# Performance work log

Hardware: AMD Instinct MI355X
Metric: run time of the kernel (lower is better)

## Reference

```python
import jax, jax.numpy as jnp
import numpy as np

MIN_NORM = 1e-15
PROJ_EPS = 4e-3  # fp32 eps used by hgcn PoincareBall


def _artanh(x):
    x = jnp.clip(x, -1.0 + 1e-7, 1.0 - 1e-7)
    return 0.5 * jnp.log((1.0 + x) / (1.0 - x))


def _norm(x):
    return jnp.maximum(jnp.linalg.norm(x, axis=-1, keepdims=True), MIN_NORM)


def proj(x, c):
    norm = _norm(x)
    maxnorm = (1.0 - PROJ_EPS) / jnp.sqrt(c)
    return jnp.where(norm > maxnorm, x / norm * maxnorm, x)


def expmap0(u, c):
    sqrt_c = jnp.sqrt(c)
    u_norm = _norm(u)
    return jnp.tanh(sqrt_c * u_norm) * u / (sqrt_c * u_norm)


def logmap0(p, c):
    sqrt_c = jnp.sqrt(c)
    p_norm = _norm(p)
    return _artanh(sqrt_c * p_norm) * p / (sqrt_c * p_norm)


def mobius_add(x, y, c):
    x2 = jnp.sum(x * x, axis=-1, keepdims=True)
    y2 = jnp.sum(y * y, axis=-1, keepdims=True)
    xy = jnp.sum(x * y, axis=-1, keepdims=True)
    num = (1.0 + 2.0 * c * xy + c * y2) * x + (1.0 - c * x2) * y
    denom = 1.0 + 2.0 * c * xy + c * c * x2 * y2
    return num / jnp.maximum(denom, MIN_NORM)


def mobius_matvec(m, x, c):
    sqrt_c = jnp.sqrt(c)
    x_norm = _norm(x)
    mx = x @ m.T  # [N, out]
    mx_norm = _norm(mx)
    res_c = jnp.tanh(mx_norm / x_norm * _artanh(sqrt_c * x_norm)) * mx / (mx_norm * sqrt_c)
    cond = jnp.all(mx == 0.0, axis=-1, keepdims=True)
    return jnp.where(cond, jnp.zeros_like(res_c), res_c)


def setup_inputs() -> dict:
    key = jax.random.key(0)
    k1, k2, k3 = jax.random.split(key, 3)
    N, D = 8192, 256
    c = 1.0
    x = 0.05 * jax.random.normal(k1, (N, D), dtype=jnp.float32)
    x = proj(x, c)  # valid points on the Poincare ball
    # sparse-ish row-normalized adjacency, materialized densely
    a = (jax.random.uniform(k2, (N, N)) < 0.004).astype(jnp.float32)
    a = a + jnp.eye(N, dtype=jnp.float32)
    adj = a / jnp.sum(a, axis=-1, keepdims=True)
    gain = np.sqrt(2.0)
    bound = gain * np.sqrt(6.0 / (D + D))  # xavier_uniform with gain sqrt(2)
    weight = jax.random.uniform(k3, (D, D), minval=-bound, maxval=bound, dtype=jnp.float32)
    bias = jnp.zeros((D,), dtype=jnp.float32)
    return {"x": x, "adj": adj, "weight": weight, "bias": bias}


def reference(x, adj, weight, bias):
    c_in = jnp.float32(1.0)
    c_out = jnp.float32(1.0)
    # HypLinear (dropout=0, eval mode)
    mv = mobius_matvec(weight, x, c_in)
    res = proj(mv, c_in)
    hyp_bias = proj(expmap0(bias[None, :], c_in), c_in)  # proj_tan0 is identity
    h = proj(mobius_add(res, hyp_bias, c_in), c_in)
    # HypAgg (use_att=False): tangent-space neighborhood aggregation
    x_tangent = logmap0(h, c_in)
    support_t = adj @ x_tangent
    h = proj(expmap0(support_t, c_in), c_in)
    # HypAct
    xt = jax.nn.relu(logmap0(h, c_in))
    h = proj(expmap0(xt, c_out), c_out)
    return (h, adj)
```

## Files before the change

### kernel.cpp

```cpp
#include <hip/hip_runtime.h>
#include <hip/hip_bf16.h>

#define N_NODES 8192
#define D_DIM   256

typedef __attribute__((ext_vector_type(8))) short short8v;
typedef __attribute__((ext_vector_type(4))) float f32x4;

__device__ __forceinline__ float artanh_clip(float x) {
    x = fminf(x, 1.0f - 1e-7f);
    return 0.5f * logf((1.0f + x) / (1.0f - x));
}

__device__ __forceinline__ ushort4 cvt4_bf16(float4 v) {
    ushort4 b;
    b.x = __bfloat16_as_ushort(__float2bfloat16(v.x));
    b.y = __bfloat16_as_ushort(__float2bfloat16(v.y));
    b.z = __bfloat16_as_ushort(__float2bfloat16(v.z));
    b.w = __bfloat16_as_ushort(__float2bfloat16(v.w));
    return b;
}

__global__ void k0_bias(const float* __restrict__ bias, float* __restrict__ hbg) {
    __shared__ float sp[4];
    __shared__ float s_g;
    int t = threadIdx.x;
    float u = bias[t];
    float v = u * u;
    #pragma unroll
    for (int o = 1; o < 64; o <<= 1) v += __shfl_xor(v, o);
    if ((t & 63) == 0) sp[t >> 6] = v;
    __syncthreads();
    if (t == 0) {
        float s  = sp[0] + sp[1] + sp[2] + sp[3];
        float un = fmaxf(sqrtf(s), 1e-15f);
        float t1 = tanhf(un);
        s_g = (t1 > 0.996f) ? (0.996f / un) : (t1 / un);
    }
    __syncthreads();
    float hb = s_g * u;
    hbg[t] = hb;
    float v2 = hb * hb;
    #pragma unroll
    for (int o = 1; o < 64; o <<= 1) v2 += __shfl_xor(v2, o);
    if ((t & 63) == 0) sp[t >> 6] = v2;
    __syncthreads();
    if (t == 0) hbg[256] = sp[0] + sp[1] + sp[2] + sp[3];
}

__global__ __launch_bounds__(256) void k1_hyplinear(
    const float* __restrict__ x, const float* __restrict__ W,
    const float* __restrict__ hbg, __hip_bfloat16* __restrict__ xtT)
{
    __shared__ __align__(16) float sx[32][260];
    __shared__ __align__(16) float sw[256][68];
    __shared__ float s_xn[32], s_P[32], s_Q[32];
    __shared__ float s_hb[256];
    __shared__ float s_b2;

    const int t  = threadIdx.x;
    const int r0 = blockIdx.x * 32;

    {
        int row = t >> 3, c0 = (t & 7) * 32;
        const float4* src = (const float4*)(x + (r0 + row) * 256 + c0);
        float4* dst = (float4*)(&sx[row][c0]);
        #pragma unroll
        for (int i = 0; i < 8; i++) dst[i] = src[i];
    }
    s_hb[t] = hbg[t];
    if (t == 0) s_b2 = hbg[256];
    __syncthreads();

    {
        int r = t >> 3, j = t & 7;
        float s2 = 0.f;
        #pragma unroll
        for (int i = 0; i < 32; i++) { float v = sx[r][j * 32 + i]; s2 += v * v; }
        s2 += __shfl_xor(s2, 1); s2 += __shfl_xor(s2, 2); s2 += __shfl_xor(s2, 4);
        if (j == 0) s_xn[r] = s2;
    }

    float acc[32];
    #pragma unroll
    for (int r = 0; r < 32; r++) acc[r] = 0.f;

    for (int kc = 0; kc < 4; kc++) {
        __syncthreads();
        int d0 = t >> 4, j4 = (t & 15) * 4;
        #pragma unroll
        for (int i = 0; i < 16; i++) {
            int d = d0 + i * 16;
            float4 w4 = *(const float4*)(W + d * 256 + kc * 64 + j4);
            *(float4*)(&sw[d][j4]) = w4;
        }
        __syncthreads();
        #pragma unroll
        for (int kk = 0; kk < 16; kk++) {
            float4 w4 = *(const float4*)(&sw[t][kk * 4]);
            #pragma unroll
            for (int r = 0; r < 32; r++) {
                float4 x4 = *(const float4*)(&sx[r][kc * 64 + kk * 4]);
                acc[r] += w4.x * x4.x + w4.y * x4.y + w4.z * x4.z + w4.w * x4.w;
            }
        }
    }
    __syncthreads();
    #pragma unroll
    for (int r = 0; r < 32; r++) sx[r][t] = acc[r];
    __syncthreads();

    {
        int r = t >> 3, j = t & 7;
        float s2 = 0.f, dt = 0.f;
        #pragma unroll
        for (int i = 0; i < 32; i++) {
            float v = sx[r][j * 32 + i];
            s2 += v * v;
            dt += v * s_hb[j * 32 + i];
        }
        s2 += __shfl_xor(s2, 1); s2 += __shfl_xor(s2, 2); s2 += __shfl_xor(s2, 4);
        dt += __shfl_xor(dt, 1); dt += __shfl_xor(dt, 2); dt += __shfl_xor(dt, 4);
        if (j == 0) {
            float b2  = s_b2;
            float xn  = fmaxf(sqrtf(s_xn[r]), 1e-15f);
            float mx2 = s2;
            float mxn = fmaxf(sqrtf(mx2), 1e-15f);
            float at = artanh_clip(xn);
            float tt = tanhf(mxn / xn * at);
            float fr = tt / mxn;
            if (tt > 0.996f) fr = 0.996f / mxn;
            float mvn = fminf(tt, 0.996f);
            float x2  = mvn * mvn;
            float xy  = fr * dt;
            float cA  = 1.0f + 2.0f * xy + b2;
            float cB  = 1.0f - x2;
            float den = fmaxf(1.0f + 2.0f * xy + x2 * b2, 1e-15f);
            float P0 = cA * fr / den;
            float Q0 = cB / den;
            float hn = sqrtf(fmaxf(P0 * P0 * mx2 + 2.0f * P0 * Q0 * dt + Q0 * Q0 * b2, 0.0f));
            hn = fmaxf(hn, 1e-15f);
            float pf  = (hn > 0.996f) ? (0.996f / hn) : 1.0f;
            float hnp = fminf(hn, 0.996f);
            float lam = artanh_clip(hnp) / hnp;
            s_P[r] = lam * pf * P0;
            s_Q[r] = lam * pf * Q0;
        }
    }
    __syncthreads();

    {
        float hb = s_hb[t];
        unsigned int pk[16];
        #pragma unroll
        for (int r = 0; r < 32; r += 2) {
            float a0 = s_P[r]     * acc[r]     + s_Q[r]     * hb;
            float a1 = s_P[r + 1] * acc[r + 1] + s_Q[r + 1] * hb;
            unsigned int lo = (unsigned int)__bfloat16_as_ushort(__float2bfloat16(a0));
            unsigned int hi = (unsigned int)__bfloat16_as_ushort(__float2bfloat16(a1));
            pk[r >> 1] = lo | (hi << 16);
        }
        uint4* dst = (uint4*)(xtT + t * 8192 + r0);
        #pragma unroll
        for (int i = 0; i < 4; i++)
            dst[i] = make_uint4(pk[4 * i], pk[4 * i + 1], pk[4 * i + 2], pk[4 * i + 3]);
    }
}

__global__ __launch_bounds__(512) void k2_agg(
    const float* __restrict__ adj,
    const __hip_bfloat16* __restrict__ xtT,
    float* __restrict__ out_h,
    float* __restrict__ out_adj)
{
    __shared__ __align__(16) __hip_bfloat16 As[2][32][72];
    __shared__ __align__(16) float sup[32][260];
    __shared__ float sF[32];

    const int t    = threadIdx.x;
    const int lane = t & 63;
    const int wave = t >> 6;
    const int wr   = wave >> 2;
    const int wc   = wave & 3;
    const int m0   = blockIdx.x * 32;

    const int srow = t >> 4;
    const int scol = (t & 15) * 4;

    f32x4 acc[2][4];
    #pragma unroll
    for (int i = 0; i < 2; i++)
        #pragma unroll
        for (int j = 0; j < 4; j++) acc[i][j] = (f32x4){0.f, 0.f, 0.f, 0.f};

    const int arow = lane & 15;
    const int acol = wr * 32 + 8 * (lane >> 4);
    const int brow = wc * 64 + (lane & 15);
    const int bk   = wr * 32 + 8 * (lane >> 4);
    const __hip_bfloat16* bptr = xtT + brow * 8192 + bk;

    {
        int g = (m0 + srow) * 8192 + scol;
        float4 v = *(const float4*)(adj + g);
        *(float4*)(out_adj + g) = v;
        *(ushort4*)(&As[0][srow][scol]) = cvt4_bf16(v);
    }
    __syncthreads();

    int cur = 0;
    for (int kt = 0; kt < 128; kt++) {
        const int k0 = kt * 64;
        float4 v;
        const bool has_next = (kt + 1 < 128);
        if (has_next)
            v = *(const float4*)(adj + (m0 + srow) * 8192 + k0 + 64 + scol);

        const __hip_bfloat16* bb = bptr + k0;
        short8v b0 = *(const short8v*)(bb);
        short8v b1 = *(const short8v*)(bb + 16 * 8192);
        short8v b2 = *(const short8v*)(bb + 32 * 8192);
        short8v b3 = *(const short8v*)(bb + 48 * 8192);
        short8v a0 = *(const short8v*)(&As[cur][arow][acol]);
        short8v a1 = *(const short8v*)(&As[cur][16 + arow][acol]);

        acc[0][0] = __builtin_amdgcn_mfma_f32_16x16x32_bf16(a0, b0, acc[0][0], 0, 0, 0);
        acc[0][1] = __builtin_amdgcn_mfma_f32_16x16x32_bf16(a0, b1, acc[0][1], 0, 0, 0);
        acc[0][2] = __builtin_amdgcn_mfma_f32_16x16x32_bf16(a0, b2, acc[0][2], 0, 0, 0);
        acc[0][3] = __builtin_amdgcn_mfma_f32_16x16x32_bf16(a0, b3, acc[0][3], 0, 0, 0);
        acc[1][0] = __builtin_amdgcn_mfma_f32_16x16x32_bf16(a1, b0, acc[1][0], 0, 0, 0);
        acc[1][1] = __builtin_amdgcn_mfma_f32_16x16x32_bf16(a1, b1, acc[1][1], 0, 0, 0);
        acc[1][2] = __builtin_amdgcn_mfma_f32_16x16x32_bf16(a1, b2, acc[1][2], 0, 0, 0);
        acc[1][3] = __builtin_amdgcn_mfma_f32_16x16x32_bf16(a1, b3, acc[1][3], 0, 0, 0);

        if (has_next) {
            int g = (m0 + srow) * 8192 + k0 + 64 + scol;
            *(float4*)(out_adj + g) = v;
            *(ushort4*)(&As[cur ^ 1][srow][scol]) = cvt4_bf16(v);
        }
        __syncthreads();
        cur ^= 1;
    }

    const int crow0 = 4 * (lane >> 4);
    const int ccol  = lane & 15;
    if (wr == 0) {
        #pragma unroll
        for (int mf = 0; mf < 2; mf++)
            #pragma unroll
            for (int nf = 0; nf < 4; nf++)
                #pragma unroll
                for (int q = 0; q < 4; q++)
                    sup[mf * 16 + crow0 + q][wc * 64 + nf * 16 + ccol] = acc[mf][nf][q];
    }
    __syncthreads();
    if (wr == 1) {
        #pragma unroll
        for (int mf = 0; mf < 2; mf++)
            #pragma unroll
            for (int nf = 0; nf < 4; nf++)
                #pragma unroll
                for (int q = 0; q < 4; q++)
                    sup[mf * 16 + crow0 + q][wc * 64 + nf * 16 + ccol] += acc[mf][nf][q];
    }
    __syncthreads();

    {
        int r = t >> 4, j = t & 15;
        float s2 = 0.f, sp = 0.f;
        #pragma unroll
        for (int i = 0; i < 16; i++) {
            float vv = sup[r][j * 16 + i];
            s2 += vv * vv;
            float vp = fmaxf(vv, 0.f);
            sp += vp * vp;
        }
        s2 += __shfl_xor(s2, 1); s2 += __shfl_xor(s2, 2); s2 += __shfl_xor(s2, 4); s2 += __shfl_xor(s2, 8);
        sp += __shfl_xor(sp, 1); sp += __shfl_xor(sp, 2); sp += __shfl_xor(sp, 4); sp += __shfl_xor(sp, 8);
        if (j == 0) {
            float ns = fmaxf(sqrtf(s2), 1e-15f);
            float t1 = tanhf(ns);
            float alpha = (t1 > 0.996f) ? (0.996f / ns) : (t1 / ns);
            float nh = fminf(t1, 0.996f);
            float beta = artanh_clip(nh) / nh;
            float ba = beta * alpha;
            float nxt = fmaxf(ba * sqrtf(sp), 1e-15f);
            float t2 = tanhf(nxt);
            float delta = (t2 > 0.996f) ? (0.996f / nxt) : (t2 / nxt);
            sF[r] = delta * ba;
        }
    }
    __syncthreads();
    {
        int r = t >> 4, j = t & 15;
        float F = sF[r];
        float4* dst = (float4*)(out_h + (m0 + r) * 256 + j * 16);
        #pragma unroll
        for (int i = 0; i < 4; i++) {
            float4 o;
            o.x = F * fmaxf(sup[r][j * 16 + 4 * i + 0], 0.f);
            o.y = F * fmaxf(sup[r][j * 16 + 4 * i + 1], 0.f);
            o.z = F * fmaxf(sup[r][j * 16 + 4 * i + 2], 0.f);
            o.w = F * fmaxf(sup[r][j * 16 + 4 * i + 3], 0.f);
            dst[i] = o;
        }
    }
}

extern "C" void kernel_launch(void* const* d_in, const int* in_sizes, int n_in,
                              void* d_out, int out_size, void* d_ws, size_t ws_size,
                              hipStream_t stream)
{
    const float* x    = (const float*)d_in[0];
    const float* adj  = (const float*)d_in[1];
    const float* W    = (const float*)d_in[2];
    const float* bias = (const float*)d_in[3];

    float* out_h   = (float*)d_out;
    float* out_adj = out_h + (size_t)N_NODES * D_DIM;

    __hip_bfloat16* xtT = (__hip_bfloat16*)d_ws;
    float* hbg = (float*)((char*)d_ws + (size_t)D_DIM * N_NODES * 2);

    k0_bias<<<1, 256, 0, stream>>>(bias, hbg);
    k1_hyplinear<<<256, 256, 0, stream>>>(x, W, hbg, xtT);
    k2_agg<<<256, 512, 0, stream>>>(adj, xtT, out_h, out_adj);
}
```

Measured before the change: 326.2 us.

## Load adjacency fragments directly to registers with double-buffered prefetch; halve k1 tile

```diff
diff --git a/kernel.cpp b/kernel.cpp
--- a/kernel.cpp
+++ b/kernel.cpp
@@ -12,13 +12,17 @@
     return 0.5f * logf((1.0f + x) / (1.0f - x));
 }
 
-__device__ __forceinline__ ushort4 cvt4_bf16(float4 v) {
-    ushort4 b;
-    b.x = __bfloat16_as_ushort(__float2bfloat16(v.x));
-    b.y = __bfloat16_as_ushort(__float2bfloat16(v.y));
-    b.z = __bfloat16_as_ushort(__float2bfloat16(v.z));
-    b.w = __bfloat16_as_ushort(__float2bfloat16(v.w));
-    return b;
+__device__ __forceinline__ short8v cvt8_bf16(float4 lo, float4 hi) {
+    union { ushort u[8]; short8v v; } r;
+    r.u[0] = __bfloat16_as_ushort(__float2bfloat16(lo.x));
+    r.u[1] = __bfloat16_as_ushort(__float2bfloat16(lo.y));
+    r.u[2] = __bfloat16_as_ushort(__float2bfloat16(lo.z));
+    r.u[3] = __bfloat16_as_ushort(__float2bfloat16(lo.w));
+    r.u[4] = __bfloat16_as_ushort(__float2bfloat16(hi.x));
+    r.u[5] = __bfloat16_as_ushort(__float2bfloat16(hi.y));
+    r.u[6] = __bfloat16_as_ushort(__float2bfloat16(hi.z));
+    r.u[7] = __bfloat16_as_ushort(__float2bfloat16(hi.w));
+    return r.v;
 }
 
 __global__ void k0_bias(const float* __restrict__ bias, float* __restrict__ hbg) {
@@ -52,75 +56,83 @@
     const float* __restrict__ x, const float* __restrict__ W,
     const float* __restrict__ hbg, __hip_bfloat16* __restrict__ xtT)
 {
-    __shared__ __align__(16) float sx[32][260];
-    __shared__ __align__(16) float sw[256][68];
-    __shared__ float s_xn[32], s_P[32], s_Q[32];
+    __shared__ __align__(16) float sx[16][260];
+    __shared__ __align__(16) float sw[256][36];
+    __shared__ float s_xn[16], s_P[16], s_Q[16];
     __shared__ float s_hb[256];
     __shared__ float s_b2;
 
     const int t  = threadIdx.x;
-    const int r0 = blockIdx.x * 32;
-
-    {
-        int row = t >> 3, c0 = (t & 7) * 32;
-        const float4* src = (const float4*)(x + (r0 + row) * 256 + c0);
-        float4* dst = (float4*)(&sx[row][c0]);
-        #pragma unroll
-        for (int i = 0; i < 8; i++) dst[i] = src[i];
+    const int r0 = blockIdx.x * 16;
+    const int row = t >> 4;
+    const int j16 = (t & 15) * 4;
+
+    {
+        #pragma unroll
+        for (int i = 0; i < 4; i++)
+            *(float4*)(&sx[row][j16 + 64 * i]) =
+                *(const float4*)(x + (r0 + row) * 256 + j16 + 64 * i);
     }
     s_hb[t] = hbg[t];
     if (t == 0) s_b2 = hbg[256];
     __syncthreads();
 
     {
-        int r = t >> 3, j = t & 7;
+        int r = t >> 4, j = t & 15;
         float s2 = 0.f;
         #pragma unroll
-        for (int i = 0; i < 32; i++) { float v = sx[r][j * 32 + i]; s2 += v * v; }
-        s2 += __shfl_xor(s2, 1); s2 += __shfl_xor(s2, 2); s2 += __shfl_xor(s2, 4);
+        for (int i = 0; i < 16; i++) { float v = sx[r][j + 16 * i]; s2 += v * v; }
+        s2 += __shfl_xor(s2, 1); s2 += __shfl_xor(s2, 2);
+        s2 += __shfl_xor(s2, 4); s2 += __shfl_xor(s2, 8);
         if (j == 0) s_xn[r] = s2;
     }
 
-    float acc[32];
-    #pragma unroll
-    for (int r = 0; r < 32; r++) acc[r] = 0.f;
-
-    for (int kc = 0; kc < 4; kc++) {
+    float acc[16];
+    #pragma unroll
+    for (int r = 0; r < 16; r++) acc[r] = 0.f;
+
+    for (int kc = 0; kc < 8; kc++) {
         __syncthreads();
-        int d0 = t >> 4, j4 = (t & 15) * 4;
-        #pragma unroll
-        for (int i = 0; i < 16; i++) {
-            int d = d0 + i * 16;
-            float4 w4 = *(const float4*)(W + d * 256 + kc * 64 + j4);
-            *(float4*)(&sw[d][j4]) = w4;
+        {
+            int c4 = (t & 7) * 4;
+            #pragma unroll
+            for (int i = 0; i < 8; i++) {
+                int d = i * 32 + (t >> 3);
+                *(float4*)(&sw[d][c4]) = *(const float4*)(W + d * 256 + kc * 32 + c4);
+            }
         }
         __syncthreads();
         #pragma unroll
-        for (int kk = 0; kk < 16; kk++) {
+        for (int kk = 0; kk < 8; kk++) {
             float4 w4 = *(const float4*)(&sw[t][kk * 4]);
             #pragma unroll
-            for (int r = 0; r < 32; r++) {
-                float4 x4 = *(const float4*)(&sx[r][kc * 64 + kk * 4]);
-                acc[r] += w4.x * x4.x + w4.y * x4.y + w4.z * x4.z + w4.w * x4.w;
+            for (int r = 0; r < 16; r++) {
+                float4 x4 = *(const float4*)(&sx[r][kc * 32 + kk * 4]);
+                acc[r] = fmaf(w4.x, x4.x, acc[r]);
+                acc[r] = fmaf(w4.y, x4.y, acc[r]);
+                acc[r] = fmaf(w4.z, x4.z, acc[r]);
+                acc[r] = fmaf(w4.w, x4.w, acc[r]);
             }
         }
     }
     __syncthreads();
     #pragma unroll
-    for (int r = 0; r < 32; r++) sx[r][t] = acc[r];
-    __syncthreads();
-
-    {
-        int r = t >> 3, j = t & 7;
+    for (int r = 0; r < 16; r++) sx[r][t] = acc[r];
+    __syncthreads();
+
+    {
+        int r = t >> 4, j = t & 15;
         float s2 = 0.f, dt = 0.f;
         #pragma unroll
-        for (int i = 0; i < 32; i++) {
-            float v = sx[r][j * 32 + i];
+        for (int i = 0; i < 16; i++) {
+            float v = sx[r][j + 16 * i];
             s2 += v * v;
-            dt += v * s_hb[j * 32 + i];
-        }
-        s2 += __shfl_xor(s2, 1); s2 += __shfl_xor(s2, 2); s2 += __shfl_xor(s2, 4);
-        dt += __shfl_xor(dt, 1); dt += __shfl_xor(dt, 2); dt += __shfl_xor(dt, 4);
+            dt += v * s_hb[j + 16 * i];
+        }
+        s2 += __shfl_xor(s2, 1); s2 += __shfl_xor(s2, 2);
+        s2 += __shfl_xor(s2, 4); s2 += __shfl_xor(s2, 8);
+        dt += __shfl_xor(dt, 1); dt += __shfl_xor(dt, 2);
+        dt += __shfl_xor(dt, 4); dt += __shfl_xor(dt, 8);
         if (j == 0) {
             float b2  = s_b2;
             float xn  = fmaxf(sqrtf(s_xn[r]), 1e-15f);
@@ -151,9 +163,9 @@
 
     {
         float hb = s_hb[t];
-        unsigned int pk[16];
-        #pragma unroll
-        for (int r = 0; r < 32; r += 2) {
+        unsigned int pk[8];
+        #pragma unroll
+        for (int r = 0; r < 16; r += 2) {
             float a0 = s_P[r]     * acc[r]     + s_Q[r]     * hb;
             float a1 = s_P[r + 1] * acc[r + 1] + s_Q[r + 1] * hb;
             unsigned int lo = (unsigned int)__bfloat16_as_ushort(__float2bfloat16(a0));
@@ -161,10 +173,48 @@
             pk[r >> 1] = lo | (hi << 16);
         }
         uint4* dst = (uint4*)(xtT + t * 8192 + r0);
-        #pragma unroll
-        for (int i = 0; i < 4; i++)
-            dst[i] = make_uint4(pk[4 * i], pk[4 * i + 1], pk[4 * i + 2], pk[4 * i + 3]);
-    }
+        dst[0] = make_uint4(pk[0], pk[1], pk[2], pk[3]);
+        dst[1] = make_uint4(pk[4], pk[5], pk[6], pk[7]);
+    }
+}
+
+struct Tile {
+    float4 A00, A01, A10, A11;
+    short8v B0, B1, B2, B3;
+};
+
+__device__ __forceinline__ void load_tile(Tile& T,
+    const float* aptr0, const float* aptr1, const __hip_bfloat16* bptr, int k0)
+{
+    T.A00 = *(const float4*)(aptr0 + k0);
+    T.A01 = *(const float4*)(aptr0 + k0 + 4);
+    T.A10 = *(const float4*)(aptr1 + k0);
+    T.A11 = *(const float4*)(aptr1 + k0 + 4);
+    T.B0  = *(const short8v*)(bptr + k0);
+    T.B1  = *(const short8v*)(bptr + 16 * 8192 + k0);
+    T.B2  = *(const short8v*)(bptr + 32 * 8192 + k0);
+    T.B3  = *(const short8v*)(bptr + 48 * 8192 + k0);
+}
+
+__device__ __forceinline__ void consume_tile(const Tile& T, f32x4* acc,
+    bool st, float* optr0, float* optr1, int k0)
+{
+    if (st) {
+        *(float4*)(optr0 + k0)     = T.A00;
+        *(float4*)(optr0 + k0 + 4) = T.A01;
+        *(float4*)(optr1 + k0)     = T.A10;
+        *(float4*)(optr1 + k0 + 4) = T.A11;
+    }
+    short8v a0 = cvt8_bf16(T.A00, T.A01);
+    short8v a1 = cvt8_bf16(T.A10, T.A11);
+    acc[0] = __builtin_amdgcn_mfma_f32_16x16x32_bf16(a0, T.B0, acc[0], 0, 0, 0);
+    acc[1] = __builtin_amdgcn_mfma_f32_16x16x32_bf16(a0, T.B1, acc[1], 0, 0, 0);
+    acc[2] = __builtin_amdgcn_mfma_f32_16x16x32_bf16(a0, T.B2, acc[2], 0, 0, 0);
+    acc[3] = __builtin_amdgcn_mfma_f32_16x16x32_bf16(a0, T.B3, acc[3], 0, 0, 0);
+    acc[4] = __builtin_amdgcn_mfma_f32_16x16x32_bf16(a1, T.B0, acc[4], 0, 0, 0);
+    acc[5] = __builtin_amdgcn_mfma_f32_16x16x32_bf16(a1, T.B1, acc[5], 0, 0, 0);
+    acc[6] = __builtin_amdgcn_mfma_f32_16x16x32_bf16(a1, T.B2, acc[6], 0, 0, 0);
+    acc[7] = __builtin_amdgcn_mfma_f32_16x16x32_bf16(a1, T.B3, acc[7], 0, 0, 0);
 }
 
 __global__ __launch_bounds__(512) void k2_agg(
@@ -173,7 +223,6 @@
     float* __restrict__ out_h,
     float* __restrict__ out_adj)
 {
-    __shared__ __align__(16) __hip_bfloat16 As[2][32][72];
     __shared__ __align__(16) float sup[32][260];
     __shared__ float sF[32];
 
@@ -184,61 +233,32 @@
     const int wc   = wave & 3;
     const int m0   = blockIdx.x * 32;
 
-    const int srow = t >> 4;
-    const int scol = (t & 15) * 4;
-
-    f32x4 acc[2][4];
-    #pragma unroll
-    for (int i = 0; i < 2; i++)
-        #pragma unroll
-        for (int j = 0; j < 4; j++) acc[i][j] = (f32x4){0.f, 0.f, 0.f, 0.f};
-
     const int arow = lane & 15;
-    const int acol = wr * 32 + 8 * (lane >> 4);
-    const int brow = wc * 64 + (lane & 15);
-    const int bk   = wr * 32 + 8 * (lane >> 4);
-    const __hip_bfloat16* bptr = xtT + brow * 8192 + bk;
-
-    {
-        int g = (m0 + srow) * 8192 + scol;
-        float4 v = *(const float4*)(adj + g);
-        *(float4*)(out_adj + g) = v;
-        *(ushort4*)(&As[0][srow][scol]) = cvt4_bf16(v);
-    }
-    __syncthreads();
-
-    int cur = 0;
-    for (int kt = 0; kt < 128; kt++) {
-        const int k0 = kt * 64;
-        float4 v;
-        const bool has_next = (kt + 1 < 128);
-        if (has_next)
-            v = *(const float4*)(adj + (m0 + srow) * 8192 + k0 + 64 + scol);
-
-        const __hip_bfloat16* bb = bptr + k0;
-        short8v b0 = *(const short8v*)(bb);
-        short8v b1 = *(const short8v*)(bb + 16 * 8192);
-        short8v b2 = *(const short8v*)(bb + 32 * 8192);
-        short8v b3 = *(const short8v*)(bb + 48 * 8192);
-        short8v a0 = *(const short8v*)(&As[cur][arow][acol]);
-        short8v a1 = *(const short8v*)(&As[cur][16 + arow][acol]);
-
-        acc[0][0] = __builtin_amdgcn_mfma_f32_16x16x32_bf16(a0, b0, acc[0][0], 0, 0, 0);
-        acc[0][1] = __builtin_amdgcn_mfma_f32_16x16x32_bf16(a0, b1, acc[0][1], 0, 0, 0);
-        acc[0][2] = __builtin_amdgcn_mfma_f32_16x16x32_bf16(a0, b2, acc[0][2], 0, 0, 0);
-        acc[0][3] = __builtin_amdgcn_mfma_f32_16x16x32_bf16(a0, b3, acc[0][3], 0, 0, 0);
-        acc[1][0] = __builtin_amdgcn_mfma_f32_16x16x32_bf16(a1, b0, acc[1][0], 0, 0, 0);
-        acc[1][1] = __builtin_amdgcn_mfma_f32_16x16x32_bf16(a1, b1, acc[1][1], 0, 0, 0);
-        acc[1][2] = __builtin_amdgcn_mfma_f32_16x16x32_bf16(a1, b2, acc[1][2], 0, 0, 0);
-        acc[1][3] = __builtin_amdgcn_mfma_f32_16x16x32_bf16(a1, b3, acc[1][3], 0, 0, 0);
-
-        if (has_next) {
-            int g = (m0 + srow) * 8192 + k0 + 64 + scol;
-            *(float4*)(out_adj + g) = v;
-            *(ushort4*)(&As[cur ^ 1][srow][scol]) = cvt4_bf16(v);
-        }
-        __syncthreads();
-        cur ^= 1;
+    const int g8   = 8 * (lane >> 4);
+    const int acol = wr * 32 + g8;
+
+    const float* aptr0 = adj + (m0 + arow) * 8192 + acol;
+    const float* aptr1 = aptr0 + 16 * 8192;
+    float* optr0 = out_adj + (m0 + arow) * 8192 + acol;
+    float* optr1 = optr0 + 16 * 8192;
+    const __hip_bfloat16* bptr = xtT + (wc * 64 + arow) * 8192 + wr * 32 + g8;
+    const bool st = (wc == 0);
+
+    f32x4 acc[8];
+    #pragma unroll
+    for (int i = 0; i < 8; i++) acc[i] = (f32x4){0.f, 0.f, 0.f, 0.f};
+
+    Tile Ta, Tb;
+    load_tile(Ta, aptr0, aptr1, bptr, 0);
+
+    for (int kt = 0; kt < 128; kt += 2) {
+        load_tile(Tb, aptr0, aptr1, bptr, (kt + 1) * 64);
+        consume_tile(Ta, acc, st, optr0, optr1, kt * 64);
+        __builtin_amdgcn_s_barrier();
+        if (kt + 2 < 128)
+            load_tile(Ta, aptr0, aptr1, bptr, (kt + 2) * 64);
+        consume_tile(Tb, acc, st, optr0, optr1, (kt + 1) * 64);
+        __builtin_amdgcn_s_barrier();
     }
 
     const int crow0 = 4 * (lane >> 4);
@@ -250,7 +270,7 @@
             for (int nf = 0; nf < 4; nf++)
                 #pragma unroll
                 for (int q = 0; q < 4; q++)
-                    sup[mf * 16 + crow0 + q][wc * 64 + nf * 16 + ccol] = acc[mf][nf][q];
+                    sup[mf * 16 + crow0 + q][wc * 64 + nf * 16 + ccol] = acc[mf * 4 + nf][q];
     }
     __syncthreads();
     if (wr == 1) {
@@ -260,7 +280,7 @@
             for (int nf = 0; nf < 4; nf++)
                 #pragma unroll
                 for (int q = 0; q < 4; q++)
-                    sup[mf * 16 + crow0 + q][wc * 64 + nf * 16 + ccol] += acc[mf][nf][q];
+                    sup[mf * 16 + crow0 + q][wc * 64 + nf * 16 + ccol] += acc[mf * 4 + nf][q];
     }
     __syncthreads();
 
@@ -269,7 +289,7 @@
         float s2 = 0.f, sp = 0.f;
         #pragma unroll
         for (int i = 0; i < 16; i++) {
-            float vv = sup[r][j * 16 + i];
+            float vv = sup[r][j + 16 * i];
             s2 += vv * vv;
             float vp = fmaxf(vv, 0.f);
             sp += vp * vp;
@@ -322,6 +342,6 @@
     float* hbg = (float*)((char*)d_ws + (size_t)D_DIM * N_NODES * 2);
 
     k0_bias<<<1, 256, 0, stream>>>(bias, hbg);
-    k1_hyplinear<<<256, 256, 0, stream>>>(x, W, hbg, xtT);
+    k1_hyplinear<<<512, 256, 0, stream>>>(x, W, hbg, xtT);
     k2_agg<<<256, 512, 0, stream>>>(adj, xtT, out_h, out_adj);
 }
```

New measurement: 430.5 us. 1.32x slower.

## Split-K the adjacency aggregation with atomics and a separate epilogue kernel

Applied to the files above, without the earlier changes.

```diff
diff --git a/kernel.cpp b/kernel.cpp
--- a/kernel.cpp
+++ b/kernel.cpp
@@ -52,75 +52,78 @@
     const float* __restrict__ x, const float* __restrict__ W,
     const float* __restrict__ hbg, __hip_bfloat16* __restrict__ xtT)
 {
-    __shared__ __align__(16) float sx[32][260];
-    __shared__ __align__(16) float sw[256][68];
-    __shared__ float s_xn[32], s_P[32], s_Q[32];
+    __shared__ __align__(16) float sw[256][36];
+    __shared__ __align__(16) float smx[16][260];
+    __shared__ float s_xn[16], s_P[16], s_Q[16];
     __shared__ float s_hb[256];
     __shared__ float s_b2;
 
     const int t  = threadIdx.x;
-    const int r0 = blockIdx.x * 32;
-
-    {
-        int row = t >> 3, c0 = (t & 7) * 32;
-        const float4* src = (const float4*)(x + (r0 + row) * 256 + c0);
-        float4* dst = (float4*)(&sx[row][c0]);
-        #pragma unroll
-        for (int i = 0; i < 8; i++) dst[i] = src[i];
-    }
+    const int r0 = blockIdx.x * 16;
+
     s_hb[t] = hbg[t];
     if (t == 0) s_b2 = hbg[256];
-    __syncthreads();
 
     {
-        int r = t >> 3, j = t & 7;
+        int r = t >> 4, j = t & 15;
+        const float* xp = x + (r0 + r) * 256 + j * 16;
         float s2 = 0.f;
         #pragma unroll
-        for (int i = 0; i < 32; i++) { float v = sx[r][j * 32 + i]; s2 += v * v; }
-        s2 += __shfl_xor(s2, 1); s2 += __shfl_xor(s2, 2); s2 += __shfl_xor(s2, 4);
+        for (int i = 0; i < 4; i++) {
+            float4 v = *(const float4*)(xp + 4 * i);
+            s2 += v.x * v.x + v.y * v.y + v.z * v.z + v.w * v.w;
+        }
+        s2 += __shfl_xor(s2, 1); s2 += __shfl_xor(s2, 2);
+        s2 += __shfl_xor(s2, 4); s2 += __shfl_xor(s2, 8);
         if (j == 0) s_xn[r] = s2;
     }
 
-    float acc[32];
-    #pragma unroll
-    for (int r = 0; r < 32; r++) acc[r] = 0.f;
-
-    for (int kc = 0; kc < 4; kc++) {
+    float acc[16];
+    #pragma unroll
+    for (int r = 0; r < 16; r++) acc[r] = 0.f;
+
+    for (int kc = 0; kc < 8; kc++) {
         __syncthreads();
-        int d0 = t >> 4, j4 = (t & 15) * 4;
-        #pragma unroll
-        for (int i = 0; i < 16; i++) {
-            int d = d0 + i * 16;
-            float4 w4 = *(const float4*)(W + d * 256 + kc * 64 + j4);
-            *(float4*)(&sw[d][j4]) = w4;
+        {
+            int c4 = (t & 7) * 4;
+            #pragma unroll
+            for (int i = 0; i < 8; i++) {
+                int d = i * 32 + (t >> 3);
+                *(float4*)(&sw[d][c4]) = *(const float4*)(W + d * 256 + kc * 32 + c4);
+            }
         }
         __syncthreads();
         #pragma unroll
-        for (int kk = 0; kk < 16; kk++) {
+        for (int kk = 0; kk < 8; kk++) {
             float4 w4 = *(const float4*)(&sw[t][kk * 4]);
             #pragma unroll
-            for (int r = 0; r < 32; r++) {
-                float4 x4 = *(const float4*)(&sx[r][kc * 64 + kk * 4]);
-                acc[r] += w4.x * x4.x + w4.y * x4.y + w4.z * x4.z + w4.w * x4.w;
+            for (int r = 0; r < 16; r++) {
+                const float4 xv = *(const float4*)(x + (r0 + r) * 256 + kc * 32 + kk * 4);
+                acc[r] = fmaf(xv.x, w4.x, acc[r]);
+                acc[r] = fmaf(xv.y, w4.y, acc[r]);
+                acc[r] = fmaf(xv.z, w4.z, acc[r]);
+                acc[r] = fmaf(xv.w, w4.w, acc[r]);
             }
         }
     }
     __syncthreads();
     #pragma unroll
-    for (int r = 0; r < 32; r++) sx[r][t] = acc[r];
+    for (int r = 0; r < 16; r++) smx[r][t] = acc[r];
     __syncthreads();
 
     {
-        int r = t >> 3, j = t & 7;
+        int r = t >> 4, j = t & 15;
         float s2 = 0.f, dt = 0.f;
         #pragma unroll
-        for (int i = 0; i < 32; i++) {
-            float v = sx[r][j * 32 + i];
+        for (int i = 0; i < 16; i++) {
+            float v = smx[r][j + 16 * i];
             s2 += v * v;
-            dt += v * s_hb[j * 32 + i];
-        }
-        s2 += __shfl_xor(s2, 1); s2 += __shfl_xor(s2, 2); s2 += __shfl_xor(s2, 4);
-        dt += __shfl_xor(dt, 1); dt += __shfl_xor(dt, 2); dt += __shfl_xor(dt, 4);
+            dt += v * s_hb[j + 16 * i];
+        }
+        s2 += __shfl_xor(s2, 1); s2 += __shfl_xor(s2, 2);
+        s2 += __shfl_xor(s2, 4); s2 += __shfl_xor(s2, 8);
+        dt += __shfl_xor(dt, 1); dt += __shfl_xor(dt, 2);
+        dt += __shfl_xor(dt, 4); dt += __shfl_xor(dt, 8);
         if (j == 0) {
             float b2  = s_b2;
             float xn  = fmaxf(sqrtf(s_xn[r]), 1e-15f);
@@ -151,9 +154,9 @@
 
     {
         float hb = s_hb[t];
-        unsigned int pk[16];
-        #pragma unroll
-        for (int r = 0; r < 32; r += 2) {
+        unsigned int pk[8];
+        #pragma unroll
+        for (int r = 0; r < 16; r += 2) {
             float a0 = s_P[r]     * acc[r]     + s_Q[r]     * hb;
             float a1 = s_P[r + 1] * acc[r + 1] + s_Q[r + 1] * hb;
             unsigned int lo = (unsigned int)__bfloat16_as_ushort(__float2bfloat16(a0));
@@ -161,9 +164,8 @@
             pk[r >> 1] = lo | (hi << 16);
         }
         uint4* dst = (uint4*)(xtT + t * 8192 + r0);
-        #pragma unroll
-        for (int i = 0; i < 4; i++)
-            dst[i] = make_uint4(pk[4 * i], pk[4 * i + 1], pk[4 * i + 2], pk[4 * i + 3]);
+        dst[0] = make_uint4(pk[0], pk[1], pk[2], pk[3]);
+        dst[1] = make_uint4(pk[4], pk[5], pk[6], pk[7]);
     }
 }
 
@@ -174,48 +176,44 @@
     float* __restrict__ out_adj)
 {
     __shared__ __align__(16) __hip_bfloat16 As[2][32][72];
-    __shared__ __align__(16) float sup[32][260];
-    __shared__ float sF[32];
-
-    const int t    = threadIdx.x;
-    const int lane = t & 63;
-    const int wave = t >> 6;
-    const int wr   = wave >> 2;
-    const int wc   = wave & 3;
-    const int m0   = blockIdx.x * 32;
+
+    const int t     = threadIdx.x;
+    const int lane  = t & 63;
+    const int wave  = t >> 6;
+    const int wr    = wave >> 2;
+    const int wc    = wave & 3;
+    const int bx    = blockIdx.x;
+    const int m0    = (bx >> 2) * 32;
+    const int kbase = (bx & 3) * 2048;
 
     const int srow = t >> 4;
     const int scol = (t & 15) * 4;
-
-    f32x4 acc[2][4];
-    #pragma unroll
-    for (int i = 0; i < 2; i++)
-        #pragma unroll
-        for (int j = 0; j < 4; j++) acc[i][j] = (f32x4){0.f, 0.f, 0.f, 0.f};
+    const float* astage = adj     + (m0 + srow) * 8192 + kbase + scol;
+    float*       ostage = out_adj + (m0 + srow) * 8192 + kbase + scol;
 
     const int arow = lane & 15;
-    const int acol = wr * 32 + 8 * (lane >> 4);
-    const int brow = wc * 64 + (lane & 15);
-    const int bk   = wr * 32 + 8 * (lane >> 4);
-    const __hip_bfloat16* bptr = xtT + brow * 8192 + bk;
+    const int g8   = 8 * (lane >> 4);
+    const int acol = wr * 32 + g8;
+    const __hip_bfloat16* bptr = xtT + (wc * 64 + arow) * 8192 + kbase + wr * 32 + g8;
+
+    f32x4 acc[8];
+    #pragma unroll
+    for (int i = 0; i < 8; i++) acc[i] = (f32x4){0.f, 0.f, 0.f, 0.f};
 
     {
-        int g = (m0 + srow) * 8192 + scol;
-        float4 v = *(const float4*)(adj + g);
-        *(float4*)(out_adj + g) = v;
+        float4 v = *(const float4*)(astage);
+        *(float4*)(ostage) = v;
         *(ushort4*)(&As[0][srow][scol]) = cvt4_bf16(v);
     }
     __syncthreads();
 
-    int cur = 0;
-    for (int kt = 0; kt < 128; kt++) {
-        const int k0 = kt * 64;
+    for (int kt = 0; kt < 32; kt++) {
+        const int cur = kt & 1;
+        const bool hn = (kt + 1 < 32);
         float4 v;
-        const bool has_next = (kt + 1 < 128);
-        if (has_next)
-            v = *(const float4*)(adj + (m0 + srow) * 8192 + k0 + 64 + scol);
-
-        const __hip_bfloat16* bb = bptr + k0;
+        if (hn) v = *(const float4*)(astage + (kt + 1) * 64);
+
+        const __hip_bfloat16* bb = bptr + kt * 64;
         short8v b0 = *(const short8v*)(bb);
         short8v b1 = *(const short8v*)(bb + 16 * 8192);
         short8v b2 = *(const short8v*)(bb + 32 * 8192);
@@ -223,86 +221,72 @@
         short8v a0 = *(const short8v*)(&As[cur][arow][acol]);
         short8v a1 = *(const short8v*)(&As[cur][16 + arow][acol]);
 
-        acc[0][0] = __builtin_amdgcn_mfma_f32_16x16x32_bf16(a0, b0, acc[0][0], 0, 0, 0);
-        acc[0][1] = __builtin_amdgcn_mfma_f32_16x16x32_bf16(a0, b1, acc[0][1], 0, 0, 0);
-        acc[0][2] = __builtin_amdgcn_mfma_f32_16x16x32_bf16(a0, b2, acc[0][2], 0, 0, 0);
-        acc[0][3] = __builtin_amdgcn_mfma_f32_16x16x32_bf16(a0, b3, acc[0][3], 0, 0, 0);
-        acc[1][0] = __builtin_amdgcn_mfma_f32_16x16x32_bf16(a1, b0, acc[1][0], 0, 0, 0);
-        acc[1][1] = __builtin_amdgcn_mfma_f32_16x16x32_bf16(a1, b1, acc[1][1], 0, 0, 0);
-        acc[1][2] = __builtin_amdgcn_mfma_f32_16x16x32_bf16(a1, b2, acc[1][2], 0, 0, 0);
-        acc[1][3] = __builtin_amdgcn_mfma_f32_16x16x32_bf16(a1, b3, acc[1][3], 0, 0, 0);
-
-        if (has_next) {
-            int g = (m0 + srow) * 8192 + k0 + 64 + scol;
-            *(float4*)(out_adj + g) = v;
+        acc[0] = __builtin_amdgcn_mfma_f32_16x16x32_bf16(a0, b0, acc[0], 0, 0, 0);
+        acc[1] = __builtin_amdgcn_mfma_f32_16x16x32_bf16(a0, b1, acc[1], 0, 0, 0);
+        acc[2] = __builtin_amdgcn_mfma_f32_16x16x32_bf16(a0, b2, acc[2], 0, 0, 0);
+        acc[3] = __builtin_amdgcn_mfma_f32_16x16x32_bf16(a0, b3, acc[3], 0, 0, 0);
+        acc[4] = __builtin_amdgcn_mfma_f32_16x16x32_bf16(a1, b0, acc[4], 0, 0, 0);
+        acc[5] = __builtin_amdgcn_mfma_f32_16x16x32_bf16(a1, b1, acc[5], 0, 0, 0);
+        acc[6] = __builtin_amdgcn_mfma_f32_16x16x32_bf16(a1, b2, acc[6], 0, 0, 0);
+        acc[7] = __builtin_amdgcn_mfma_f32_16x16x32_bf16(a1, b3, acc[7], 0, 0, 0);
+
+        if (hn) {
+            *(float4*)(ostage + (kt + 1) * 64) = v;
             *(ushort4*)(&As[cur ^ 1][srow][scol]) = cvt4_bf16(v);
         }
         __syncthreads();
-        cur ^= 1;
     }
 
     const int crow0 = 4 * (lane >> 4);
     const int ccol  = lane & 15;
-    if (wr == 0) {
-        #pragma unroll
-        for (int mf = 0; mf < 2; mf++)
+    #pragma unroll
+    for (int mf = 0; mf < 2; mf++)
+        #pragma unroll
+        for (int nf = 0; nf < 4; nf++)
             #pragma unroll
-            for (int nf = 0; nf < 4; nf++)
-                #pragma unroll
-                for (int q = 0; q < 4; q++)
-                    sup[mf * 16 + crow0 + q][wc * 64 + nf * 16 + ccol] = acc[mf][nf][q];
-    }
-    __syncthreads();
-    if (wr == 1) {
-        #pragma unroll
-        for (int mf = 0; mf < 2; mf++)
-            #pragma unroll
-            for (int nf = 0; nf < 4; nf++)
-                #pragma unroll
-                for (int q = 0; q < 4; q++)
-                    sup[mf * 16 + crow0 + q][wc * 64 + nf * 16 + ccol] += acc[mf][nf][q];
-    }
-    __syncthreads();
-
-    {
-        int r = t >> 4, j = t & 15;
-        float s2 = 0.f, sp = 0.f;
-        #pragma unroll
-        for (int i = 0; i < 16; i++) {
-            float vv = sup[r][j * 16 + i];
-            s2 += vv * vv;
-            float vp = fmaxf(vv, 0.f);
-            sp += vp * vp;
-        }
-        s2 += __shfl_xor(s2, 1); s2 += __shfl_xor(s2, 2); s2 += __shfl_xor(s2, 4); s2 += __shfl_xor(s2, 8);
-        sp += __shfl_xor(sp, 1); sp += __shfl_xor(sp, 2); sp += __shfl_xor(sp, 4); sp += __shfl_xor(sp, 8);
-        if (j == 0) {
-            float ns = fmaxf(sqrtf(s2), 1e-15f);
-            float t1 = tanhf(ns);
-            float alpha = (t1 > 0.996f) ? (0.996f / ns) : (t1 / ns);
-            float nh = fminf(t1, 0.996f);
-            float beta = artanh_clip(nh) / nh;
-            float ba = beta * alpha;
-            float nxt = fmaxf(ba * sqrtf(sp), 1e-15f);
-            float t2 = tanhf(nxt);
-            float delta = (t2 > 0.996f) ? (0.996f / nxt) : (t2 / nxt);
-            sF[r] = delta * ba;
-        }
-    }
-    __syncthreads();
-    {
-        int r = t >> 4, j = t & 15;
-        float F = sF[r];
-        float4* dst = (float4*)(out_h + (m0 + r) * 256 + j * 16);
-        #pragma unroll
-        for (int i = 0; i < 4; i++) {
-            float4 o;
-            o.x = F * fmaxf(sup[r][j * 16 + 4 * i + 0], 0.f);
-            o.y = F * fmaxf(sup[r][j * 16 + 4 * i + 1], 0.f);
-            o.z = F * fmaxf(sup[r][j * 16 + 4 * i + 2], 0.f);
-            o.w = F * fmaxf(sup[r][j * 16 + 4 * i + 3], 0.f);
-            dst[i] = o;
-        }
+            for (int q = 0; q < 4; q++)
+                atomicAdd(out_h + (m0 + mf * 16 + crow0 + q) * 256 + wc * 64 + nf * 16 + ccol,
+                          acc[mf * 4 + nf][q]);
+}
+
+__global__ __launch_bounds__(256) void k3_epilogue(float* __restrict__ h) {
+    const int t = threadIdx.x;
+    const int r = blockIdx.x * 16 + (t >> 4);
+    const int j = t & 15;
+    float* p = h + r * 256 + j * 16;
+
+    float4 v[4];
+    float s2 = 0.f, sp = 0.f;
+    #pragma unroll
+    for (int i = 0; i < 4; i++) {
+        v[i] = *(const float4*)(p + 4 * i);
+        s2 += v[i].x * v[i].x + v[i].y * v[i].y + v[i].z * v[i].z + v[i].w * v[i].w;
+        float px = fmaxf(v[i].x, 0.f), py = fmaxf(v[i].y, 0.f);
+        float pz = fmaxf(v[i].z, 0.f), pw = fmaxf(v[i].w, 0.f);
+        sp += px * px + py * py + pz * pz + pw * pw;
+    }
+    s2 += __shfl_xor(s2, 1); s2 += __shfl_xor(s2, 2); s2 += __shfl_xor(s2, 4); s2 += __shfl_xor(s2, 8);
+    sp += __shfl_xor(sp, 1); sp += __shfl_xor(sp, 2); sp += __shfl_xor(sp, 4); sp += __shfl_xor(sp, 8);
+
+    float ns = fmaxf(sqrtf(s2), 1e-15f);
+    float t1 = tanhf(ns);
+    float alpha = (t1 > 0.996f) ? (0.996f / ns) : (t1 / ns);
+    float nh = fminf(t1, 0.996f);
+    float beta = artanh_clip(nh) / nh;
+    float ba = beta * alpha;
+    float nxt = fmaxf(ba * sqrtf(sp), 1e-15f);
+    float t2 = tanhf(nxt);
+    float delta = (t2 > 0.996f) ? (0.996f / nxt) : (t2 / nxt);
+    float F = delta * ba;
+
+    #pragma unroll
+    for (int i = 0; i < 4; i++) {
+        float4 o;
+        o.x = F * fmaxf(v[i].x, 0.f);
+        o.y = F * fmaxf(v[i].y, 0.f);
+        o.z = F * fmaxf(v[i].z, 0.f);
+        o.w = F * fmaxf(v[i].w, 0.f);
+        *(float4*)(p + 4 * i) = o;
     }
 }
 
@@ -322,6 +306,8 @@
     float* hbg = (float*)((char*)d_ws + (size_t)D_DIM * N_NODES * 2);
 
     k0_bias<<<1, 256, 0, stream>>>(bias, hbg);
-    k1_hyplinear<<<256, 256, 0, stream>>>(x, W, hbg, xtT);
-    k2_agg<<<256, 512, 0, stream>>>(adj, xtT, out_h, out_adj);
-}
+    k1_hyplinear<<<512, 256, 0, stream>>>(x, W, hbg, xtT);
+    hipMemsetAsync(out_h, 0, (size_t)N_NODES * D_DIM * sizeof(float), stream);
+    k2_agg<<<1024, 512, 0, stream>>>(adj, xtT, out_h, out_adj);
+    k3_epilogue<<<512, 256, 0, stream>>>(out_h);
+}
```

New measurement: 304.8 us. 1.07x faster.
